# Kernel optimization log

Measured on AMD Instinct MI355X. Metric: run time of the kernel, lower is better.

## Reference

```python
import jax, jax.numpy as jnp
import numpy as np
from jax import lax

B, T, I = 64, 256, 256
H, C, H2, O = 1024, 128, 256, 1


def lstm(x, h0, c0, Wih, Whh, bih, bhh):
    """Single-layer LSTM, PyTorch gate order (i, f, g, o).
    x: [B, T, I]; h0/c0: [B, H]. Returns (h_seq [T,B,H], h_T, c_T)."""
    def step(carry, xt):
        h, c = carry
        gates = xt @ Wih.T + h @ Whh.T + bih + bhh  # [B, 4H]
        i, f, g, o = jnp.split(gates, 4, axis=-1)
        i = jax.nn.sigmoid(i)
        f = jax.nn.sigmoid(f)
        g = jnp.tanh(g)
        o = jax.nn.sigmoid(o)
        c = f * c + i * g
        h = o * jnp.tanh(c)
        return (h, c), h
    (hT, cT), hs = lax.scan(step, (h0, c0), jnp.swapaxes(x, 0, 1))
    return hs, hT, cT


def setup_inputs() -> dict:
    key = jax.random.key(0)
    ks = jax.random.split(key, 16)
    s_ih = 1.0 / np.sqrt(I)
    s_hh = 1.0 / np.sqrt(H)
    inp = {
        "x": jax.random.normal(ks[0], (B, T, I), dtype=jnp.float32),
        "additional": jax.random.normal(ks[1], (B, C), dtype=jnp.float32),
        "enc_Wih": jax.random.normal(ks[2], (4 * H, I), dtype=jnp.float32) * s_ih,
        "enc_Whh": jax.random.normal(ks[3], (4 * H, H), dtype=jnp.float32) * s_hh,
        "enc_bih": jnp.ones((4 * H,), dtype=jnp.float32),
        "enc_bhh": jnp.ones((4 * H,), dtype=jnp.float32),
        "dec_Wih": jax.random.normal(ks[4], (4 * H, I), dtype=jnp.float32) * s_ih,
        "dec_Whh": jax.random.normal(ks[5], (4 * H, H), dtype=jnp.float32) * s_hh,
        "dec_bih": jnp.ones((4 * H,), dtype=jnp.float32),
        "dec_bhh": jnp.ones((4 * H,), dtype=jnp.float32),
        "fcc_W": jax.random.normal(ks[6], (H2, C), dtype=jnp.float32) * np.sqrt(2.0 / C),
        "fcc_b": jnp.zeros((H2,), dtype=jnp.float32),
        "fc_W": jax.random.normal(ks[7], (O, H + H2), dtype=jnp.float32) * 0.01,
        "fc_b": jnp.zeros((O,), dtype=jnp.float32),
        "prelu_a": jnp.float32(0.25),
    }
    return inp


def reference(x, additional, enc_Wih, enc_Whh, enc_bih, enc_bhh,
              dec_Wih, dec_Whh, dec_bih, dec_bhh,
              fcc_W, fcc_b, fc_W, fc_b, prelu_a):
    b = x.shape[0]
    h0 = jnp.zeros((b, H), dtype=x.dtype)
    c0 = jnp.zeros((b, H), dtype=x.dtype)
    # Encoder over full sequence.
    _, eh, ec = lstm(x, h0, c0, enc_Wih, enc_Whh, enc_bih, enc_bhh)
    # Decoder: the per-timestep Python loop feeding x[:, t, :] with carried
    # state is exactly an LSTM scan over the same sequence, starting from the
    # encoder final state.
    _, dh, _ = lstm(x, eh, ec, dec_Wih, dec_Whh, dec_bih, dec_bhh)
    # Tail MLP: PReLU(fc_concat(additional)), concat with final hidden, fc.
    a = additional @ fcc_W.T + fcc_b
    a = jnp.where(a >= 0, a, prelu_a * a)
    concatenated = jnp.concatenate((dh, a), axis=1)  # [B, H+H2]
    return concatenated @ fc_W.T + fc_b
```

## Files before the change

kernel.cpp:

```cpp
#include <hip/hip_runtime.h>
#include <cmath>

typedef _Float16 f16;
typedef _Float16 f16x8 __attribute__((ext_vector_type(8)));
typedef _Float16 f16x4 __attribute__((ext_vector_type(4)));
typedef float f32x4 __attribute__((ext_vector_type(4)));
typedef unsigned long long u64;

#define H_DIM 1024
#define I_DIMM 256
#define B_DIM 64
#define T_DIM 256
#define K_DIM 1280
#define NBLK 128
#define SLABSZ (NBLK * 64 * 8)
#define FSTRIDE 64

__global__ __launch_bounds__(256) void conv_w_kernel(const float* __restrict__ Whh,
                                                     const float* __restrict__ Wih,
                                                     f16* __restrict__ W16) {
    const int r = blockIdx.x;
    const int tid = threadIdx.x;
    const float* hh = Whh + (size_t)r * H_DIM;
    const float* ih = Wih + (size_t)r * I_DIMM;
    f16* dst = W16 + (size_t)r * K_DIM;
    for (int k = tid; k < K_DIM; k += 256)
        dst[k] = (f16)(k < H_DIM ? hh[k] : ih[k - H_DIM]);
}

__global__ __launch_bounds__(256) void conv_x_kernel(const float* __restrict__ x,
                                                     f16* __restrict__ x16, int n4) {
    const int i = blockIdx.x * 256 + threadIdx.x;
    if (i < n4) {
        float4 v = ((const float4*)x)[i];
        f16x4 o;
        o[0] = (f16)v.x; o[1] = (f16)v.y; o[2] = (f16)v.z; o[3] = (f16)v.w;
        ((f16x4*)x16)[i] = o;
    }
}

__device__ __forceinline__ float fsig(float x) {
    return __builtin_amdgcn_rcpf(1.f + __builtin_amdgcn_exp2f(-1.442695041f * x));
}
__device__ __forceinline__ float ftanh(float x) {
    return 1.f - 2.f * __builtin_amdgcn_rcpf(1.f + __builtin_amdgcn_exp2f(2.885390082f * x));
}

__global__ __launch_bounds__(512, 1) void lstm_persistent(
    f16* __restrict__ hX,
    const f16* __restrict__ x16,
    const f16* __restrict__ W16e,
    const f16* __restrict__ W16d,
    const float* __restrict__ enc_bih, const float* __restrict__ enc_bhh,
    const float* __restrict__ dec_bih, const float* __restrict__ dec_bhh,
    unsigned* __restrict__ flags)
{
    __shared__ __align__(16) f16 lds_w[2][40][64][8];
    __shared__ float gpart[4][64][34];
    __shared__ __align__(16) f16 h_lds[64][8];

    const int tid  = threadIdx.x;
    const int blk  = blockIdx.x;
    const int w    = tid >> 6;
    const int bh   = w >> 2;
    const int kq   = w & 3;
    const int lane = tid & 63;
    const int n    = lane & 15;
    const int kg   = lane >> 4;
    const int kg8  = kg * 8;

    const int pl   = lane & 31;
    const unsigned* fpoll = &flags[(((pl >> 2) * 16) + kq * 4 + (pl & 3)) * FSTRIDE];

    int rW[2];
    #pragma unroll
    for (int ct = 0; ct < 2; ++ct) {
        const int gc = ct * 16 + n;
        rW[ct] = (gc >> 3) * H_DIM + blk * 8 + (gc & 7);
    }

    const int ab   = tid >> 3;
    const int aj   = tid & 7;
    const int acol = blk * 8 + aj;

    float c_reg = 0.f;
    unsigned stepv = 0;

    #pragma unroll 1
    for (int phase = 0; phase < 2; ++phase) {
        const f16* W  = phase ? W16d : W16e;
        const float* bi = phase ? dec_bih : enc_bih;
        const float* bhp = phase ? dec_bhh : enc_bhh;

        float bsum[4];
        #pragma unroll
        for (int g = 0; g < 4; ++g)
            bsum[g] = bi[g * H_DIM + acol] + bhp[g * H_DIM + acol];

        {
            const int it0 = bh * 5;
            #pragma unroll 1
            for (int i = 0; i < 5; ++i) {
                const int c = (it0 + i) * 4 + kq;
                #pragma unroll
                for (int ct = 0; ct < 2; ++ct)
                    *(f16x8*)&lds_w[ct][c][lane][0] =
                        *(const f16x8*)(W + (size_t)rW[ct] * K_DIM + c * 32 + kg8);
            }
        }
        __syncthreads();

        #pragma unroll 1
        for (int t = 0; t < T_DIM; ++t) {
            const f16* slab_in  = hX + (size_t)(t & 1) * SLABSZ;
            f16*       slab_out = hX + (size_t)((t + 1) & 1) * SLABSZ;
            const f16* xt = x16 + (size_t)t * I_DIMM;

            f32x4 acc[2][2];
            #pragma unroll
            for (int ct = 0; ct < 2; ++ct)
                #pragma unroll
                for (int btl = 0; btl < 2; ++btl)
                    acc[ct][btl] = (f32x4){0.f, 0.f, 0.f, 0.f};

            #pragma unroll
            for (int it = 8; it < 10; ++it) {
                const int c  = it * 4 + kq;
                const int xo = c * 32 - 1024 + kg8;
                f16x8 wf0 = *(const f16x8*)&lds_w[0][c][lane][0];
                f16x8 wf1 = *(const f16x8*)&lds_w[1][c][lane][0];
                #pragma unroll
                for (int btl = 0; btl < 2; ++btl) {
                    const int btg = bh * 2 + btl;
                    f16x8 a = *(const f16x8*)(xt + (size_t)(n + 16 * btg) * (T_DIM * I_DIMM) + xo);
                    acc[0][btl] = __builtin_amdgcn_mfma_f32_16x16x32_f16(a, wf0, acc[0][btl], 0, 0, 0);
                    acc[1][btl] = __builtin_amdgcn_mfma_f32_16x16x32_f16(a, wf1, acc[1][btl], 0, 0, 0);
                }
            }

            while (true) {
                unsigned v = __hip_atomic_load(fpoll, __ATOMIC_RELAXED,
                                               __HIP_MEMORY_SCOPE_AGENT);
                if (__all(v >= stepv)) break;
                __builtin_amdgcn_s_sleep(1);
            }

            u64 hb[32];
            #pragma unroll
            for (int it = 0; it < 8; ++it) {
                const int pb = it * 16 + kq * 4 + kg;
                #pragma unroll
                for (int btl = 0; btl < 2; ++btl) {
                    const int btg = bh * 2 + btl;
                    const u64* p = (const u64*)slab_in + (((size_t)pb * 64 + n + 16 * btg) << 1);
                    hb[(it * 2 + btl) * 2 + 0] =
                        __hip_atomic_load(p,     __ATOMIC_RELAXED, __HIP_MEMORY_SCOPE_AGENT);
                    hb[(it * 2 + btl) * 2 + 1] =
                        __hip_atomic_load(p + 1, __ATOMIC_RELAXED, __HIP_MEMORY_SCOPE_AGENT);
                }
            }
            __builtin_amdgcn_sched_barrier(0);

            #pragma unroll
            for (int it = 0; it < 8; ++it) {
                const int c = it * 4 + kq;
                f16x8 wf0 = *(const f16x8*)&lds_w[0][c][lane][0];
                f16x8 wf1 = *(const f16x8*)&lds_w[1][c][lane][0];
                #pragma unroll
                for (int btl = 0; btl < 2; ++btl) {
                    union { u64 u[2]; f16x8 v; } U;
                    U.u[0] = hb[(it * 2 + btl) * 2 + 0];
                    U.u[1] = hb[(it * 2 + btl) * 2 + 1];
                    acc[0][btl] = __builtin_amdgcn_mfma_f32_16x16x32_f16(U.v, wf0, acc[0][btl], 0, 0, 0);
                    acc[1][btl] = __builtin_amdgcn_mfma_f32_16x16x32_f16(U.v, wf1, acc[1][btl], 0, 0, 0);
                }
            }

            #pragma unroll
            for (int ct = 0; ct < 2; ++ct)
                #pragma unroll
                for (int btl = 0; btl < 2; ++btl)
                    #pragma unroll
                    for (int r = 0; r < 4; ++r)
                        gpart[kq][(bh * 2 + btl) * 16 + kg * 4 + r][ct * 16 + n] = acc[ct][btl][r];
            __syncthreads();

            {
                float pre[4];
                #pragma unroll
                for (int g = 0; g < 4; ++g)
                    pre[g] = gpart[0][ab][g * 8 + aj] + gpart[1][ab][g * 8 + aj]
                           + gpart[2][ab][g * 8 + aj] + gpart[3][ab][g * 8 + aj] + bsum[g];
                const float i_ = fsig(pre[0]);
                const float f_ = fsig(pre[1]);
                const float g_ = ftanh(pre[2]);
                const float o_ = fsig(pre[3]);
                c_reg = f_ * c_reg + i_ * g_;
                h_lds[ab][aj] = (f16)(o_ * ftanh(c_reg));
            }
            __syncthreads();

            ++stepv;
            if (w == 0) {
                const u64* src = (const u64*)&h_lds[lane][0];
                u64 v0 = src[0], v1 = src[1];
                u64* dst = (u64*)slab_out + (((size_t)blk * 64 + lane) << 1);
                __hip_atomic_store(dst,     v0, __ATOMIC_RELAXED, __HIP_MEMORY_SCOPE_AGENT);
                __hip_atomic_store(dst + 1, v1, __ATOMIC_RELAXED, __HIP_MEMORY_SCOPE_AGENT);
                asm volatile("s_waitcnt vmcnt(0)" ::: "memory");
                if (lane == 0)
                    __hip_atomic_store(&flags[blk * FSTRIDE], stepv,
                                       __ATOMIC_RELAXED, __HIP_MEMORY_SCOPE_AGENT);
            }
        }
    }
}

__global__ __launch_bounds__(256) void tail_kernel(
    const f16* __restrict__ hX,
    const float* __restrict__ addl,
    const float* __restrict__ fccW,
    const float* __restrict__ fccb,
    const float* __restrict__ fcW,
    const float* __restrict__ fcb,
    const float* __restrict__ prelu_a,
    float* __restrict__ out)
{
    __shared__ float a_lds[256];
    __shared__ float red[256];
    const int b = blockIdx.x;
    const int t = threadIdx.x;

    float s = fccb[t];
    const float* wr = fccW + t * 128;
    const float* ar = addl + b * 128;
    #pragma unroll 4
    for (int k = 0; k < 128; ++k) s += ar[k] * wr[k];
    const float pa = *prelu_a;
    a_lds[t] = (s >= 0.f) ? s : pa * s;
    __syncthreads();

    float acc = 0.f;
    for (int k = t; k < 1024; k += 256)
        acc += (float)hX[((size_t)(k >> 3) * 64 + b) * 8 + (k & 7)] * fcW[k];
    acc += a_lds[t] * fcW[1024 + t];
    red[t] = acc;
    __syncthreads();
    for (int sft = 128; sft > 0; sft >>= 1) {
        if (t < sft) red[t] += red[t + sft];
        __syncthreads();
    }
    if (t == 0) out[b] = red[0] + fcb[0];
}

extern "C" void kernel_launch(void* const* d_in, const int* in_sizes, int n_in,
                              void* d_out, int out_size, void* d_ws, size_t ws_size,
                              hipStream_t stream)
{
    const float* x       = (const float*)d_in[0];
    const float* addl    = (const float*)d_in[1];
    const float* enc_Wih = (const float*)d_in[2];
    const float* enc_Whh = (const float*)d_in[3];
    const float* enc_bih = (const float*)d_in[4];
    const float* enc_bhh = (const float*)d_in[5];
    const float* dec_Wih = (const float*)d_in[6];
    const float* dec_Whh = (const float*)d_in[7];
    const float* dec_bih = (const float*)d_in[8];
    const float* dec_bhh = (const float*)d_in[9];
    const float* fcc_W   = (const float*)d_in[10];
    const float* fcc_b   = (const float*)d_in[11];
    const float* fc_W    = (const float*)d_in[12];
    const float* fc_b    = (const float*)d_in[13];
    const float* prelu_a = (const float*)d_in[14];

    char* wsb = (char*)d_ws;
    const size_t W16_BYTES  = (size_t)4 * H_DIM * K_DIM * sizeof(f16);
    const size_t X16_BYTES  = (size_t)B_DIM * T_DIM * I_DIMM * sizeof(f16);
    const size_t SLAB_BYTES = (size_t)SLABSZ * sizeof(f16);

    f16* W16e = (f16*)wsb;                      wsb += W16_BYTES;
    f16* W16d = (f16*)wsb;                      wsb += W16_BYTES;
    f16* x16  = (f16*)wsb;                      wsb += X16_BYTES;
    f16* hX   = (f16*)wsb;                      wsb += 2 * SLAB_BYTES;
    unsigned* flags = (unsigned*)wsb;

    conv_w_kernel<<<4 * H_DIM, 256, 0, stream>>>(enc_Whh, enc_Wih, W16e);
    conv_w_kernel<<<4 * H_DIM, 256, 0, stream>>>(dec_Whh, dec_Wih, W16d);
    conv_x_kernel<<<(B_DIM * T_DIM * I_DIMM / 4 + 255) / 256, 256, 0, stream>>>(
        x, x16, B_DIM * T_DIM * I_DIMM / 4);
    hipMemsetAsync(hX, 0, SLAB_BYTES, stream);
    hipMemsetAsync(flags, 0, NBLK * FSTRIDE * sizeof(unsigned), stream);

    {
        void* args[] = { &hX, &x16, &W16e, &W16d,
                         &enc_bih, &enc_bhh, &dec_bih, &dec_bhh, &flags };
        hipLaunchCooperativeKernel((void*)lstm_persistent, dim3(NBLK), dim3(512),
                                   args, 0, stream);
    }

    tail_kernel<<<64, 256, 0, stream>>>(hX, addl, fcc_W, fcc_b, fc_W, fc_b,
                                        prelu_a, (float*)d_out);
}
```

Baseline: 2.300 ms.

## Replace post-activation barrier with per-wave h publish and LDS arrival counter

```diff
diff --git a/kernel.cpp b/kernel.cpp
--- a/kernel.cpp
+++ b/kernel.cpp
@@ -56,8 +56,9 @@
     unsigned* __restrict__ flags)
 {
     __shared__ __align__(16) f16 lds_w[2][40][64][8];
-    __shared__ float gpart[4][64][34];
+    __shared__ float gpart[2][4][64][34];
     __shared__ __align__(16) f16 h_lds[64][8];
+    __shared__ unsigned arrv;
 
     const int tid  = threadIdx.x;
     const int blk  = blockIdx.x;
@@ -79,12 +80,14 @@
         rW[ct] = (gc >> 3) * H_DIM + blk * 8 + (gc & 7);
     }
 
-    const int ab   = tid >> 3;
-    const int aj   = tid & 7;
+    const int ab   = w * 8 + (lane >> 3);
+    const int aj   = lane & 7;
     const int acol = blk * 8 + aj;
 
     float c_reg = 0.f;
     unsigned stepv = 0;
+
+    if (tid == 0) arrv = 0;
 
     #pragma unroll 1
     for (int phase = 0; phase < 2; ++phase) {
@@ -115,6 +118,7 @@
             const f16* slab_in  = hX + (size_t)(t & 1) * SLABSZ;
             f16*       slab_out = hX + (size_t)((t + 1) & 1) * SLABSZ;
             const f16* xt = x16 + (size_t)t * I_DIMM;
+            const int  gp = t & 1;
 
             f32x4 acc[2][2];
             #pragma unroll
@@ -122,6 +126,9 @@
                 #pragma unroll
                 for (int btl = 0; btl < 2; ++btl)
                     acc[ct][btl] = (f32x4){0.f, 0.f, 0.f, 0.f};
+
+            unsigned vflag = __hip_atomic_load(fpoll, __ATOMIC_RELAXED,
+                                               __HIP_MEMORY_SCOPE_AGENT);
 
             #pragma unroll
             for (int it = 8; it < 10; ++it) {
@@ -138,11 +145,13 @@
                 }
             }
 
-            while (true) {
-                unsigned v = __hip_atomic_load(fpoll, __ATOMIC_RELAXED,
-                                               __HIP_MEMORY_SCOPE_AGENT);
-                if (__all(v >= stepv)) break;
-                __builtin_amdgcn_s_sleep(1);
+            if (!__all(vflag >= stepv)) {
+                while (true) {
+                    vflag = __hip_atomic_load(fpoll, __ATOMIC_RELAXED,
+                                              __HIP_MEMORY_SCOPE_AGENT);
+                    if (__all(vflag >= stepv)) break;
+                    __builtin_amdgcn_s_sleep(1);
+                }
             }
 
             u64 hb[32];
@@ -182,15 +191,17 @@
                 for (int btl = 0; btl < 2; ++btl)
                     #pragma unroll
                     for (int r = 0; r < 4; ++r)
-                        gpart[kq][(bh * 2 + btl) * 16 + kg * 4 + r][ct * 16 + n] = acc[ct][btl][r];
+                        gpart[gp][kq][(bh * 2 + btl) * 16 + kg * 4 + r][ct * 16 + n] = acc[ct][btl][r];
             __syncthreads();
+
+            ++stepv;
 
             {
                 float pre[4];
                 #pragma unroll
                 for (int g = 0; g < 4; ++g)
-                    pre[g] = gpart[0][ab][g * 8 + aj] + gpart[1][ab][g * 8 + aj]
-                           + gpart[2][ab][g * 8 + aj] + gpart[3][ab][g * 8 + aj] + bsum[g];
+                    pre[g] = gpart[gp][0][ab][g * 8 + aj] + gpart[gp][1][ab][g * 8 + aj]
+                           + gpart[gp][2][ab][g * 8 + aj] + gpart[gp][3][ab][g * 8 + aj] + bsum[g];
                 const float i_ = fsig(pre[0]);
                 const float f_ = fsig(pre[1]);
                 const float g_ = ftanh(pre[2]);
@@ -198,17 +209,15 @@
                 c_reg = f_ * c_reg + i_ * g_;
                 h_lds[ab][aj] = (f16)(o_ * ftanh(c_reg));
             }
-            __syncthreads();
-
-            ++stepv;
-            if (w == 0) {
-                const u64* src = (const u64*)&h_lds[lane][0];
-                u64 v0 = src[0], v1 = src[1];
-                u64* dst = (u64*)slab_out + (((size_t)blk * 64 + lane) << 1);
-                __hip_atomic_store(dst,     v0, __ATOMIC_RELAXED, __HIP_MEMORY_SCOPE_AGENT);
-                __hip_atomic_store(dst + 1, v1, __ATOMIC_RELAXED, __HIP_MEMORY_SCOPE_AGENT);
-                asm volatile("s_waitcnt vmcnt(0)" ::: "memory");
-                if (lane == 0)
+            if (lane < 16) {
+                u64 v = *(const u64*)&h_lds[w * 8 + (lane >> 1)][(lane & 1) * 4];
+                u64* dst = (u64*)slab_out + (size_t)blk * 128 + w * 16 + lane;
+                __hip_atomic_store(dst, v, __ATOMIC_RELAXED, __HIP_MEMORY_SCOPE_AGENT);
+            }
+            asm volatile("s_waitcnt vmcnt(0)" ::: "memory");
+            if (lane == 0) {
+                unsigned old = atomicAdd(&arrv, 1u);
+                if (old == 8u * stepv - 1u)
                     __hip_atomic_store(&flags[blk * FSTRIDE], stepv,
                                        __ATOMIC_RELAXED, __HIP_MEMORY_SCOPE_AGENT);
             }
```

After: 2.669 ms. 16.0% more time.
